# Optimization experiments

Hardware: AMD Instinct MI355X
Metric: run time of the kernel (lower is better)

## Reference

```python
import jax, jax.numpy as jnp
import numpy as np

N, DIM, HEADS, DHEAD = 4096, 1024, 16, 64
INNER = HEADS * DHEAD


def setup_inputs() -> dict:
    key = jax.random.key(0)
    ks = jax.random.split(key, 6)
    s_in = 1.0 / np.sqrt(DIM)
    s_inner = 1.0 / np.sqrt(INNER)
    return {
        "x": jax.random.normal(ks[0], (N, DIM), dtype=jnp.float32),
        # weights stored as (in, out) so y = x @ W
        "Wq": jax.random.uniform(ks[1], (DIM, INNER), jnp.float32, -s_in, s_in),
        "Wk": jax.random.uniform(ks[2], (DIM, INNER), jnp.float32, -s_in, s_in),
        "Wv": jax.random.uniform(ks[3], (DIM, INNER), jnp.float32, -s_in, s_in),
        "Wo": jax.random.uniform(ks[4], (INNER, DIM), jnp.float32, -s_inner, s_inner),
        "bo": jax.random.uniform(ks[5], (DIM,), jnp.float32, -s_inner, s_inner),
    }


def reference(x, Wq, Wk, Wv, Wo, bo):
    scale = DHEAD ** -0.5
    # [n, h, d] -> [h, n, d]
    q = (x @ Wq).reshape(N, HEADS, DHEAD).transpose(1, 0, 2)
    k = (x @ Wk).reshape(N, HEADS, DHEAD).transpose(1, 0, 2)
    v = (x @ Wv).reshape(N, HEADS, DHEAD).transpose(1, 0, 2)
    dots = jnp.einsum("hnd,hmd->hnm", q, k) * scale  # [h, n, n]
    attn = jax.nn.softmax(dots, axis=-1)
    out = jnp.einsum("hnm,hmd->hnd", attn, v)  # [h, n, d]
    out = out.transpose(1, 0, 2).reshape(N, INNER)
    return out @ Wo + bo
```

## Files before the change

kernel.cpp:

```cpp
#include <hip/hip_runtime.h>
#include <cstdint>
#include <cstddef>

typedef _Float16 f16;
typedef _Float16 f16x8 __attribute__((ext_vector_type(8)));
typedef _Float16 f16x4 __attribute__((ext_vector_type(4)));
typedef __fp16 fp16x2 __attribute__((ext_vector_type(2)));
typedef float floatx4 __attribute__((ext_vector_type(4)));
typedef float floatx16 __attribute__((ext_vector_type(16)));

constexpr int SEQ = 4096;
constexpr int DIM = 1024;
constexpr int NHEAD = 16;
constexpr int DH = 64;

#define QSCALE 0.18033688011112042f

__device__ __forceinline__ void async16(void* lds, const void* g) {
  __builtin_amdgcn_global_load_lds(
      (__attribute__((address_space(1))) void*)g,
      (__attribute__((address_space(3))) void*)lds, 16, 0, 0);
}

__device__ __forceinline__ uint32_t pk2(float a, float b) {
  union { fp16x2 h; uint32_t u; } c;
  c.h = __builtin_amdgcn_cvt_pkrtz(a, b);
  return c.u;
}

__device__ __forceinline__ float dot2acc(uint32_t packed, float acc) {
#if __has_builtin(__builtin_amdgcn_fdot2)
  union { uint32_t u; fp16x2 h; } c; c.u = packed;
  fp16x2 one2; one2.x = (__fp16)1.0f; one2.y = (__fp16)1.0f;
  return __builtin_amdgcn_fdot2(c.h, one2, acc, false);
#else
  union { uint32_t u; fp16x2 h; } c; c.u = packed;
  return acc + (float)c.h.x + (float)c.h.y;
#endif
}


__global__ void cvt_x(const float* __restrict__ x, f16* __restrict__ xh) {
  int i = (blockIdx.x * 256 + threadIdx.x) * 4;
  float4 v = *(const float4*)(x + i);
  f16x4 o;
  o.x = (f16)v.x; o.y = (f16)v.y; o.z = (f16)v.z; o.w = (f16)v.w;
  *(f16x4*)(xh + i) = o;
}

__global__ void transpose_cvt(const float* __restrict__ w0, const float* __restrict__ w1,
                              const float* __restrict__ w2, const float* __restrict__ w3,
                              f16* __restrict__ o0, f16* __restrict__ o1,
                              f16* __restrict__ o2, f16* __restrict__ o3) {
  __shared__ float tile[32][33];
  int z = blockIdx.z;
  const float* W = (z == 0) ? w0 : (z == 1) ? w1 : (z == 2) ? w2 : w3;
  f16* O = (z == 0) ? o0 : (z == 1) ? o1 : (z == 2) ? o2 : o3;
  int tx = threadIdx.x, ty = threadIdx.y;
  int xc = blockIdx.x * 32 + tx;
  for (int i = ty; i < 32; i += 8)
    tile[i][tx] = W[(size_t)(blockIdx.y * 32 + i) * DIM + xc];
  __syncthreads();
  int xo = blockIdx.y * 32 + tx;
  for (int i = ty; i < 32; i += 8)
    O[(size_t)(blockIdx.x * 32 + i) * DIM + xo] = (f16)tile[tx][i];
}

__global__ __launch_bounds__(256, 3) void gemm_qkv(
    const f16* __restrict__ xh, const f16* __restrict__ wqt,
    const f16* __restrict__ wkt, const f16* __restrict__ wvt,
    f16* __restrict__ q_ws, f16* __restrict__ k_ws, f16* __restrict__ vt_ws) {
  __shared__ f16 smem[16896];
  f16* a_lds = smem;
  f16* b_lds = smem + 4096;
  const int tid = threadIdx.x;
  const int lane = tid & 63, l16 = lane & 15, quad = lane >> 4;
  const int w = tid >> 6, wr = w >> 1, wc = w & 1;
  const int m0 = blockIdx.x * 128, n0 = blockIdx.y * 128;
  const int z = blockIdx.z;
  const f16* Bt = (z == 0) ? wqt : (z == 1) ? wkt : wvt;

  floatx4 acc[4][4];
#pragma unroll
  for (int mt = 0; mt < 4; ++mt)
#pragma unroll
    for (int nt = 0; nt < 4; ++nt) acc[mt][nt] = (floatx4){0.f, 0.f, 0.f, 0.f};

  for (int k0 = 0; k0 < DIM; k0 += 32) {
#pragma unroll
    for (int rnd = 0; rnd < 2; ++rnd) {
      int e = (rnd * 256 + tid) * 8;
      int cb = e >> 10, r = (e >> 3) & 127;
      async16(a_lds + e, xh + (size_t)(m0 + r) * DIM + k0 + cb * 8);
      async16(b_lds + e, Bt + (size_t)(n0 + r) * DIM + k0 + cb * 8);
    }
    __syncthreads();
    f16x8 af[4], bq[4];
#pragma unroll
    for (int mt = 0; mt < 4; ++mt)
      af[mt] = *(const f16x8*)(a_lds + quad * 1024 + (wr * 64 + mt * 16 + l16) * 8);
#pragma unroll
    for (int nt = 0; nt < 4; ++nt)
      bq[nt] = *(const f16x8*)(b_lds + quad * 1024 + (wc * 64 + nt * 16 + l16) * 8);
#pragma unroll
    for (int mt = 0; mt < 4; ++mt)
#pragma unroll
      for (int nt = 0; nt < 4; ++nt)
        acc[mt][nt] = __builtin_amdgcn_mfma_f32_16x16x32_f16(af[mt], bq[nt], acc[mt][nt], 0, 0, 0);
    __syncthreads();
  }

  if (z < 2) {
#pragma unroll
    for (int mt = 0; mt < 4; ++mt)
#pragma unroll
      for (int nt = 0; nt < 4; ++nt)
#pragma unroll
        for (int r = 0; r < 4; ++r) {
          int m = m0 + wr * 64 + mt * 16 + quad * 4 + r;
          int c = n0 + wc * 64 + nt * 16 + l16;
          float v = acc[mt][nt][r];
          if (z == 0)
            q_ws[(size_t)((c >> 6) * SEQ + m) * DH + (c & 63)] = (f16)(v * QSCALE);
          else
            k_ws[(size_t)((c >> 6) * SEQ + m) * DH + (c & 63)] = (f16)v;
        }
  } else {
#pragma unroll
    for (int mt = 0; mt < 4; ++mt)
#pragma unroll
      for (int nt = 0; nt < 4; ++nt)
#pragma unroll
        for (int r = 0; r < 4; ++r) {
          int cl = wc * 64 + nt * 16 + l16;
          int ml = wr * 64 + mt * 16 + quad * 4 + r;
          smem[cl * 132 + ml] = (f16)acc[mt][nt][r];
        }
    __syncthreads();
#pragma unroll
    for (int it = 0; it < 8; ++it) {
      int idx = it * 256 + tid;
      int cl = idx >> 4, mp = (idx & 15) * 8;
      f16x4 lo = *(const f16x4*)(smem + cl * 132 + mp);
      f16x4 hi4 = *(const f16x4*)(smem + cl * 132 + mp + 4);
      f16x8 v8;
#pragma unroll
      for (int j = 0; j < 4; ++j) { v8[j] = lo[j]; v8[4 + j] = hi4[j]; }
      *(f16x8*)(vt_ws + (size_t)(n0 + cl) * SEQ + m0 + mp) = v8;
    }
  }
}

__global__ __launch_bounds__(256, 4) void attn_kernel(
    const f16* __restrict__ qg, const f16* __restrict__ kg,
    const f16* __restrict__ vtg, f16* __restrict__ po, float* __restrict__ ps) {
  __shared__ f16 smem[16384];

  const int tid = threadIdx.x;
  const int w = tid >> 6, lane = tid & 63, l32 = lane & 31;
  const int hi = lane >> 5;

  const int pid = blockIdx.x + 32 * (blockIdx.y + 16 * blockIdx.z);
  const int vid = (pid & 7) * 128 + (pid >> 3);
  const int qt = vid & 31, h = (vid >> 5) & 15, half = vid >> 9;

  const int q0 = qt * 128 + w * 32;

  f16x8 qf[4];
#pragma unroll
  for (int kf = 0; kf < 4; ++kf)
    qf[kf] = *(const f16x8*)(qg + (size_t)(h * SEQ + q0 + l32) * DH + kf * 16 + hi * 8);

  floatx16 oacc[2];
  oacc[0] = (floatx16)0.f; oacc[1] = (floatx16)0.f;
  float ssum = 0.f;

  const f16* kg_h = kg + (size_t)h * SEQ * DH;
  const f16* vt_h = vtg + (size_t)h * DH * SEQ;
  const int kb0 = half * (SEQ / 128);
  constexpr int NT = SEQ / 128;

  {
    const f16* ks = kg_h + (size_t)(kb0 * 64) * DH;
    const f16* vs = vt_h + kb0 * 64;
#pragma unroll
    for (int rnd = 0; rnd < 2; ++rnd) {
      int e = (rnd * 256 + tid) * 8;
      int cb = e >> 9, r = (e >> 3) & 63;
      async16(smem + e, ks + (size_t)r * DH + cb * 8);
      async16(smem + 4096 + e, vs + (size_t)r * SEQ + cb * 8);
    }
  }

  for (int i = 0; i < NT; ++i) {
    f16* k_lds = smem + (i & 1) * 8192;
    f16* v_lds = k_lds + 4096;
    if (i + 1 < NT) {
      f16* kn = smem + ((i + 1) & 1) * 8192;
      const f16* ks = kg_h + (size_t)((kb0 + i + 1) * 64) * DH;
      const f16* vs = vt_h + (kb0 + i + 1) * 64;
#pragma unroll
      for (int rnd = 0; rnd < 2; ++rnd) {
        int e = (rnd * 256 + tid) * 8;
        int cb = e >> 9, r = (e >> 3) & 63;
        async16(kn + e, ks + (size_t)r * DH + cb * 8);
        async16(kn + 4096 + e, vs + (size_t)r * SEQ + cb * 8);
      }
      asm volatile("s_waitcnt vmcnt(4)" ::: "memory");
    } else {
      asm volatile("s_waitcnt vmcnt(0)" ::: "memory");
    }
    __builtin_amdgcn_s_barrier();
    asm volatile("" ::: "memory");

#pragma unroll
    for (int kb = 0; kb < 2; ++kb) {
      floatx16 sacc = (floatx16)0.f;
      __builtin_amdgcn_s_setprio(1);
#pragma unroll
      for (int kf = 0; kf < 4; ++kf) {
        f16x8 kfrag = *(const f16x8*)(k_lds + (kf * 2 + hi) * 512 + (kb * 32 + l32) * 8);
        sacc = __builtin_amdgcn_mfma_f32_32x32x16_f16(kfrag, qf[kf], sacc, 0, 0, 0);
      }
      __builtin_amdgcn_s_setprio(0);
      float p[16];
#pragma unroll
      for (int r = 0; r < 16; ++r) p[r] = __builtin_amdgcn_exp2f(sacc[r]);
#pragma unroll
      for (int kh = 0; kh < 2; ++kh) {
        uint32_t d0a = pk2(p[8 * kh + 0], p[8 * kh + 1]);
        uint32_t d0b = pk2(p[8 * kh + 2], p[8 * kh + 3]);
        uint32_t d1a = pk2(p[8 * kh + 4], p[8 * kh + 5]);
        uint32_t d1b = pk2(p[8 * kh + 6], p[8 * kh + 7]);
        ssum = dot2acc(d0a, ssum);
        ssum = dot2acc(d0b, ssum);
        ssum = dot2acc(d1a, ssum);
        ssum = dot2acc(d1b, ssum);
        union { uint32_t u[4]; f16x8 v; } bu;
#if __has_builtin(__builtin_amdgcn_permlane32_swap)
        {
          auto s1 = __builtin_amdgcn_permlane32_swap(d0a, d1a, false, false);
          auto s2 = __builtin_amdgcn_permlane32_swap(d0b, d1b, false, false);
          bu.u[0] = s1[0]; bu.u[1] = s2[0]; bu.u[2] = s1[1]; bu.u[3] = s2[1];
        }
#else
        {
          uint32_t ra = (uint32_t)__shfl_xor((int)(hi ? d0a : d1a), 32);
          uint32_t rb = (uint32_t)__shfl_xor((int)(hi ? d0b : d1b), 32);
          bu.u[0] = hi ? ra : d0a;
          bu.u[1] = hi ? rb : d0b;
          bu.u[2] = hi ? d1a : ra;
          bu.u[3] = hi ? d1b : rb;
        }
#endif
        int cb = kb * 4 + kh * 2 + hi;
        __builtin_amdgcn_s_setprio(1);
#pragma unroll
        for (int dt = 0; dt < 2; ++dt) {
          f16x8 vfrag = *(const f16x8*)(v_lds + cb * 512 + (dt * 32 + l32) * 8);
          oacc[dt] = __builtin_amdgcn_mfma_f32_32x32x16_f16(vfrag, bu.v, oacc[dt], 0, 0, 0);
        }
        __builtin_amdgcn_s_setprio(0);
      }
    }
    asm volatile("" ::: "memory");
    __builtin_amdgcn_s_barrier();
    asm volatile("" ::: "memory");
  }

  ssum += __shfl_xor(ssum, 32);
  const int tileid = (half * NHEAD + h) * 32 + qt;
  if (hi == 0) ps[(size_t)tileid * 128 + w * 32 + l32] = ssum;

  f16* pob = po + (size_t)tileid * 8192;
#pragma unroll
  for (int dt = 0; dt < 2; ++dt)
#pragma unroll
    for (int r = 0; r < 16; ++r) {
      int d = dt * 32 + (r & 3) + 8 * (r >> 2) + 4 * hi;
      pob[d * 128 + w * 32 + l32] = (f16)oacc[dt][r];
    }
}

__global__ __launch_bounds__(256, 4) void combine(
    const f16* __restrict__ po, const float* __restrict__ ps, f16* __restrict__ og) {
  __shared__ float inv_s[128];
  __shared__ f16 t[128 * 68];
  const int tid = threadIdx.x;
  const int h = blockIdx.y, qt = blockIdx.x;
  const int t0 = h * 32 + qt, t1 = (NHEAD + h) * 32 + qt;
  if (tid < 128) inv_s[tid] = 1.f / (ps[(size_t)t0 * 128 + tid] + ps[(size_t)t1 * 128 + tid]);
  __syncthreads();
  const f16* b0 = po + (size_t)t0 * 8192;
  const f16* b1 = po + (size_t)t1 * 8192;
#pragma unroll
  for (int it = 0; it < 4; ++it) {
    int e = (it * 256 + tid) * 8;
    int d = e >> 7, q = e & 127;
    f16x8 a = *(const f16x8*)(b0 + e);
    f16x8 b = *(const f16x8*)(b1 + e);
#pragma unroll
    for (int j = 0; j < 8; ++j)
      t[(q + j) * 68 + d] = (f16)(((float)a[j] + (float)b[j]) * inv_s[q + j]);
  }
  __syncthreads();
#pragma unroll
  for (int it = 0; it < 4; ++it) {
    int idx = it * 256 + tid;
    int q = idx >> 3, dcol = (idx & 7) * 8;
    f16x4 lo = *(const f16x4*)(t + q * 68 + dcol);
    f16x4 hi4 = *(const f16x4*)(t + q * 68 + dcol + 4);
    f16x8 v8;
#pragma unroll
    for (int j = 0; j < 4; ++j) { v8[j] = lo[j]; v8[4 + j] = hi4[j]; }
    *(f16x8*)(og + (size_t)(qt * 128 + q) * DIM + h * DH + dcol) = v8;
  }
}

__global__ __launch_bounds__(256, 2) void gemm_o(
    const f16* __restrict__ ab, const f16* __restrict__ wot,
    const float* __restrict__ bo, float* __restrict__ out) {
  __shared__ f16 a_lds[4096];
  __shared__ f16 b_lds[2048];
  const int tid = threadIdx.x;
  const int lane = tid & 63, l16 = lane & 15, quad = lane >> 4;
  const int w = tid >> 6, wr = w >> 1, wc = w & 1;
  const int m0 = blockIdx.x * 128, n0 = blockIdx.y * 64;

  floatx4 acc[4][2];
#pragma unroll
  for (int mt = 0; mt < 4; ++mt)
#pragma unroll
    for (int nt = 0; nt < 2; ++nt) acc[mt][nt] = (floatx4){0.f, 0.f, 0.f, 0.f};

  for (int k0 = 0; k0 < DIM; k0 += 32) {
#pragma unroll
    for (int rnd = 0; rnd < 2; ++rnd) {
      int e = (rnd * 256 + tid) * 8;
      int cb = e >> 10, r = (e >> 3) & 127;
      async16(a_lds + e, ab + (size_t)(m0 + r) * DIM + k0 + cb * 8);
    }
    {
      int e = tid * 8;
      int cb = e >> 9, r = (e >> 3) & 63;
      async16(b_lds + e, wot + (size_t)(n0 + r) * DIM + k0 + cb * 8);
    }
    __syncthreads();
    f16x8 af[4], bq[2];
#pragma unroll
    for (int mt = 0; mt < 4; ++mt)
      af[mt] = *(const f16x8*)(a_lds + quad * 1024 + (wr * 64 + mt * 16 + l16) * 8);
#pragma unroll
    for (int nt = 0; nt < 2; ++nt)
      bq[nt] = *(const f16x8*)(b_lds + quad * 512 + (wc * 32 + nt * 16 + l16) * 8);
#pragma unroll
    for (int mt = 0; mt < 4; ++mt)
#pragma unroll
      for (int nt = 0; nt < 2; ++nt)
        acc[mt][nt] = __builtin_amdgcn_mfma_f32_16x16x32_f16(af[mt], bq[nt], acc[mt][nt], 0, 0, 0);
    __syncthreads();
  }

#pragma unroll
  for (int mt = 0; mt < 4; ++mt)
#pragma unroll
    for (int nt = 0; nt < 2; ++nt)
#pragma unroll
      for (int r = 0; r < 4; ++r) {
        int m = m0 + wr * 64 + mt * 16 + quad * 4 + r;
        int c = n0 + wc * 32 + nt * 16 + l16;
        out[(size_t)m * DIM + c] = acc[mt][nt][r] + bo[c];
      }
}


extern "C" void kernel_launch(void* const* d_in, const int* in_sizes, int n_in,
                              void* d_out, int out_size, void* d_ws, size_t ws_size,
                              hipStream_t stream) {
  (void)in_sizes; (void)n_in; (void)out_size; (void)ws_size;
  const float* x  = (const float*)d_in[0];
  const float* Wq = (const float*)d_in[1];
  const float* Wk = (const float*)d_in[2];
  const float* Wv = (const float*)d_in[3];
  const float* Wo = (const float*)d_in[4];
  const float* bo = (const float*)d_in[5];
  float* out = (float*)d_out;
  char* ws = (char*)d_ws;

  f16* xh    = (f16*)(ws);
  f16* wqt   = (f16*)(ws + (8u  << 20));
  f16* wkt   = (f16*)(ws + (10u << 20));
  f16* wvt   = (f16*)(ws + (12u << 20));
  f16* wot   = (f16*)(ws + (14u << 20));
  f16* q_ws  = (f16*)(ws + (16u << 20));
  f16* k_ws  = (f16*)(ws + (24u << 20));
  f16* vt_ws = (f16*)(ws + (32u << 20));
  f16* po    = (f16*)(ws + (40u << 20));
  float* ps  = (float*)(ws + (57u << 20));
  f16* aout  = xh;

  cvt_x<<<dim3(SEQ * DIM / 1024), dim3(256), 0, stream>>>(x, xh);
  transpose_cvt<<<dim3(32, 32, 4), dim3(32, 8), 0, stream>>>(Wq, Wk, Wv, Wo, wqt, wkt, wvt, wot);
  gemm_qkv<<<dim3(32, 8, 3), dim3(256), 0, stream>>>(xh, wqt, wkt, wvt, q_ws, k_ws, vt_ws);
  attn_kernel<<<dim3(SEQ / 128, NHEAD, 2), dim3(256), 0, stream>>>(q_ws, k_ws, vt_ws, po, ps);
  combine<<<dim3(SEQ / 128, NHEAD), dim3(256), 0, stream>>>(po, ps, aout);
  gemm_o<<<dim3(32, 16), dim3(256), 0, stream>>>(aout, wot, bo, out);
}
```

Measured before the change: 259.5 us.

## Double-buffer LDS tiles in QKV and output projection GEMMs

Both projection GEMMs now use two LDS buffers. Each iteration issues the async global-to-LDS loads for the next K-slice before waiting, with explicit vmcnt waits and raw barriers, so memory latency overlaps the MFMA work on the current slice. This removes the load-then-wait stall in every K iteration. In exchange the output GEMM uses more LDS, and correctness now depends on the hand-counted vmcnt values matching the number of loads the compiler emits.

Result: no change. 257.2 us (-0.9%).

```diff
diff --git a/kernel.cpp b/kernel.cpp
--- a/kernel.cpp
+++ b/kernel.cpp
@@ -71,8 +71,6 @@
     const f16* __restrict__ wkt, const f16* __restrict__ wvt,
     f16* __restrict__ q_ws, f16* __restrict__ k_ws, f16* __restrict__ vt_ws) {
   __shared__ f16 smem[16896];
-  f16* a_lds = smem;
-  f16* b_lds = smem + 4096;
   const int tid = threadIdx.x;
   const int lane = tid & 63, l16 = lane & 15, quad = lane >> 4;
   const int w = tid >> 6, wr = w >> 1, wc = w & 1;
@@ -86,15 +84,31 @@
 #pragma unroll
     for (int nt = 0; nt < 4; ++nt) acc[mt][nt] = (floatx4){0.f, 0.f, 0.f, 0.f};
 
-  for (int k0 = 0; k0 < DIM; k0 += 32) {
-#pragma unroll
-    for (int rnd = 0; rnd < 2; ++rnd) {
-      int e = (rnd * 256 + tid) * 8;
-      int cb = e >> 10, r = (e >> 3) & 127;
-      async16(a_lds + e, xh + (size_t)(m0 + r) * DIM + k0 + cb * 8);
-      async16(b_lds + e, Bt + (size_t)(n0 + r) * DIM + k0 + cb * 8);
-    }
-    __syncthreads();
+#define QKV_STAGE(t_, buf_)                                                    \
+  {                                                                            \
+    int k0_ = (t_) * 32;                                                       \
+    _Pragma("unroll")                                                          \
+    for (int rnd = 0; rnd < 2; ++rnd) {                                        \
+      int e = (rnd * 256 + tid) * 8;                                           \
+      int cb = e >> 10, r = (e >> 3) & 127;                                    \
+      async16((buf_) + e, xh + (size_t)(m0 + r) * DIM + k0_ + cb * 8);         \
+      async16((buf_) + 4096 + e, Bt + (size_t)(n0 + r) * DIM + k0_ + cb * 8);  \
+    }                                                                          \
+  }
+
+  QKV_STAGE(0, smem);
+  for (int t = 0; t < 32; ++t) {
+    f16* cur = smem + (t & 1) * 8192;
+    if (t + 1 < 32) {
+      QKV_STAGE(t + 1, smem + ((t + 1) & 1) * 8192);
+      asm volatile("s_waitcnt vmcnt(4)" ::: "memory");
+    } else {
+      asm volatile("s_waitcnt vmcnt(0)" ::: "memory");
+    }
+    __builtin_amdgcn_s_barrier();
+    asm volatile("" ::: "memory");
+    const f16* a_lds = cur;
+    const f16* b_lds = cur + 4096;
     f16x8 af[4], bq[4];
 #pragma unroll
     for (int mt = 0; mt < 4; ++mt)
@@ -107,8 +121,10 @@
 #pragma unroll
       for (int nt = 0; nt < 4; ++nt)
         acc[mt][nt] = __builtin_amdgcn_mfma_f32_16x16x32_f16(af[mt], bq[nt], acc[mt][nt], 0, 0, 0);
-    __syncthreads();
-  }
+    asm volatile("" ::: "memory");
+    __builtin_amdgcn_s_barrier();
+  }
+#undef QKV_STAGE
 
   if (z < 2) {
 #pragma unroll
@@ -320,8 +336,7 @@
 __global__ __launch_bounds__(256, 2) void gemm_o(
     const f16* __restrict__ ab, const f16* __restrict__ wot,
     const float* __restrict__ bo, float* __restrict__ out) {
-  __shared__ f16 a_lds[4096];
-  __shared__ f16 b_lds[2048];
+  __shared__ f16 smem[12288];
   const int tid = threadIdx.x;
   const int lane = tid & 63, l16 = lane & 15, quad = lane >> 4;
   const int w = tid >> 6, wr = w >> 1, wc = w & 1;
@@ -333,19 +348,35 @@
 #pragma unroll
     for (int nt = 0; nt < 2; ++nt) acc[mt][nt] = (floatx4){0.f, 0.f, 0.f, 0.f};
 
-  for (int k0 = 0; k0 < DIM; k0 += 32) {
-#pragma unroll
-    for (int rnd = 0; rnd < 2; ++rnd) {
-      int e = (rnd * 256 + tid) * 8;
-      int cb = e >> 10, r = (e >> 3) & 127;
-      async16(a_lds + e, ab + (size_t)(m0 + r) * DIM + k0 + cb * 8);
-    }
-    {
-      int e = tid * 8;
-      int cb = e >> 9, r = (e >> 3) & 63;
-      async16(b_lds + e, wot + (size_t)(n0 + r) * DIM + k0 + cb * 8);
-    }
-    __syncthreads();
+#define O_STAGE(t_, buf_)                                                      \
+  {                                                                            \
+    int k0_ = (t_) * 32;                                                       \
+    _Pragma("unroll")                                                          \
+    for (int rnd = 0; rnd < 2; ++rnd) {                                        \
+      int e = (rnd * 256 + tid) * 8;                                           \
+      int cb = e >> 10, r = (e >> 3) & 127;                                    \
+      async16((buf_) + e, ab + (size_t)(m0 + r) * DIM + k0_ + cb * 8);         \
+    }                                                                          \
+    {                                                                          \
+      int e = tid * 8;                                                         \
+      int cb = e >> 9, r = (e >> 3) & 63;                                      \
+      async16((buf_) + 4096 + e, wot + (size_t)(n0 + r) * DIM + k0_ + cb * 8); \
+    }                                                                          \
+  }
+
+  O_STAGE(0, smem);
+  for (int t = 0; t < 32; ++t) {
+    f16* cur = smem + (t & 1) * 6144;
+    if (t + 1 < 32) {
+      O_STAGE(t + 1, smem + ((t + 1) & 1) * 6144);
+      asm volatile("s_waitcnt vmcnt(3)" ::: "memory");
+    } else {
+      asm volatile("s_waitcnt vmcnt(0)" ::: "memory");
+    }
+    __builtin_amdgcn_s_barrier();
+    asm volatile("" ::: "memory");
+    const f16* a_lds = cur;
+    const f16* b_lds = cur + 4096;
     f16x8 af[4], bq[2];
 #pragma unroll
     for (int mt = 0; mt < 4; ++mt)
@@ -358,8 +389,10 @@
 #pragma unroll
       for (int nt = 0; nt < 2; ++nt)
         acc[mt][nt] = __builtin_amdgcn_mfma_f32_16x16x32_f16(af[mt], bq[nt], acc[mt][nt], 0, 0, 0);
-    __syncthreads();
-  }
+    asm volatile("" ::: "memory");
+    __builtin_amdgcn_s_barrier();
+  }
+#undef O_STAGE
 
 #pragma unroll
   for (int mt = 0; mt < 4; ++mt)
```
